# Kernel tuning notes

Measured on AMD Instinct MI355X. Metric: run time of the kernel, lower is better.

Reference implementation:

```python
import jax, jax.numpy as jnp
import numpy as np

EPS = 1e-5


def _extract3x3(x, stride=1):
    # channel-major patch extraction: output [B, C*9, Ho, Wo], each channel's 3x3 window contiguous
    B, C, H, W = x.shape
    xp = jnp.pad(x, ((0, 0), (0, 0), (1, 1), (1, 1)))
    Ho = (H + 2 - 3) // stride + 1
    Wo = (W + 2 - 3) // stride + 1
    pats = [xp[:, :, i:i + (Ho - 1) * stride + 1:stride, j:j + (Wo - 1) * stride + 1:stride]
            for i in range(3) for j in range(3)]
    return jnp.stack(pats, axis=2).reshape(B, C * 9, Ho, Wo)


def _amm(patches, centroids, lut, inv_temp):
    # patches: [B, D, H, W] channel-major, D = ncodebooks * subvec_len
    # centroids: [ncb, k, sub], lut: [ncb, k, out_channels]
    B, D, H, W = patches.shape
    ncb, k, sub = centroids.shape
    v = patches.reshape(B, ncb, sub, H * W).transpose(0, 3, 1, 2)  # [B, L, ncb, sub]
    # negative squared distance to each codeword (||v||^2 dropped: constant over k)
    scores = 2.0 * jnp.einsum('blcs,cks->blck', v, centroids) - jnp.sum(centroids * centroids, -1)[None, None]
    attn = jax.nn.softmax(scores * inv_temp, axis=-1)          # soft codeword assignment
    out = jnp.einsum('blck,cko->blo', attn, lut)                # LUT gather/sum over codebooks
    return out.transpose(0, 2, 1).reshape(B, -1, H, W)


def _bn(x, g, b):
    m = x.mean((0, 2, 3), keepdims=True)
    v = x.var((0, 2, 3), keepdims=True)
    return g[None, :, None, None] * (x - m) * jax.lax.rsqrt(v + EPS) + b[None, :, None, None]


def setup_inputs() -> dict:
    key = jax.random.key(0)
    ks = jax.random.split(key, 8)
    B, C, H, W = 32, 1024, 14, 14
    width, out_c, K = 256, 1024, 16
    return {
        'x': jax.random.normal(ks[0], (B, C, H, W), jnp.float32),
        'c1_centroids': jax.random.normal(ks[1], (C // 4, K, 4), jnp.float32),
        'c1_lut': jax.random.normal(ks[2], (C // 4, K, width), jnp.float32) * 0.05,
        'c1_invt': jnp.ones((), jnp.float32),
        'c2_centroids': jax.random.normal(ks[3], (width, K, 9), jnp.float32),
        'c2_lut': jax.random.normal(ks[4], (width, K, width), jnp.float32) * 0.05,
        'c2_invt': jnp.ones((), jnp.float32),
        'c3_centroids': jax.random.normal(ks[5], (width // 4, K, 4), jnp.float32),
        'c3_lut': jax.random.normal(ks[6], (width // 4, K, out_c), jnp.float32) * 0.05,
        'c3_invt': jnp.ones((), jnp.float32),
        'bn1_g': jnp.ones((width,), jnp.float32), 'bn1_b': jnp.zeros((width,), jnp.float32),
        'bn2_g': jnp.ones((width,), jnp.float32), 'bn2_b': jnp.zeros((width,), jnp.float32),
        'bn3_g': jnp.ones((out_c,), jnp.float32), 'bn3_b': jnp.zeros((out_c,), jnp.float32),
    }


def reference(x, c1_centroids, c1_lut, c1_invt, c2_centroids, c2_lut, c2_invt,
              c3_centroids, c3_lut, c3_invt, bn1_g, bn1_b, bn2_g, bn2_b, bn3_g, bn3_b):
    identity = x
    out = _amm(x, c1_centroids, c1_lut, c1_invt)                 # amm_conv1x1, stride 1
    out = jax.nn.relu(_bn(out, bn1_g, bn1_b))
    out = _amm(_extract3x3(out, 1), c2_centroids, c2_lut, c2_invt)  # amm_conv3x3, stride 1, pad 1
    out = jax.nn.relu(_bn(out, bn2_g, bn2_b))
    out = _amm(out, c3_centroids, c3_lut, c3_invt)               # amm_conv1x1
    out = _bn(out, bn3_g, bn3_b)
    return jax.nn.relu(out + identity)
```

## Files before the change

kernel.cpp:

```cpp
#include <hip/hip_runtime.h>
#include <hip/hip_bf16.h>

#define EPSV 1e-5f

typedef unsigned short u16;
typedef __attribute__((ext_vector_type(8))) short short8;
typedef __attribute__((ext_vector_type(4))) float f32x4;
typedef __hip_bfloat16 bf16;

__device__ __forceinline__ unsigned int pack2(float a, float b) {
  bf16 ha = __float2bfloat16(a), hb = __float2bfloat16(b);
  u16 ua, ub;
  __builtin_memcpy(&ua, &ha, 2);
  __builtin_memcpy(&ub, &hb, 2);
  return (unsigned int)ua | ((unsigned int)ub << 16);
}

typedef __attribute__((address_space(1))) const void gvoid_t;
typedef __attribute__((address_space(3))) void lvoid_t;
__device__ __forceinline__ void gload16(const void* g, void* l) {
  __builtin_amdgcn_global_load_lds((gvoid_t*)g, (lvoid_t*)l, 16, 0, 0);
}


__global__ __launch_bounds__(256) void prep_kernel(
    const float* __restrict__ x, const float* __restrict__ cent,
    const float* __restrict__ invt, u16* __restrict__ attn,
    const float* __restrict__ s1, bf16* __restrict__ d1,
    const float* __restrict__ s2, bf16* __restrict__ d2,
    const float* __restrict__ s3, bf16* __restrict__ d3)
{
  __shared__ __align__(16) float sh[7012];
  const int tid = threadIdx.x;
  if (blockIdx.x >= 1024) {
    const int bid = blockIdx.x - 1024;
    const int which = bid >> 8, sub = bid & 255;
    const float* in = (which == 0) ? s1 : (which == 1) ? s2 : s3;
    bf16* out = (which == 0) ? d1 : (which == 1) ? d2 : d3;
    const int K = (which == 2) ? 1024 : 4096;
    const int N = (which == 2) ? 1024 : 256;
    const int kt = K >> 6;
    const int bk = sub & (kt - 1), bn = sub / kt;
    const int k0 = bk * 64, n0 = bn * 64;
    float* t = sh;
    for (int idx = tid; idx < 4096; idx += 256) {
      int r = idx >> 6, c = idx & 63;
      t[r * 65 + c] = in[(size_t)(k0 + r) * N + n0 + c];
    }
    __syncthreads();
    for (int idx = tid; idx < 4096; idx += 256) {
      int r = idx >> 6, c = idx & 63;
      out[(size_t)(n0 + r) * K + k0 + c] = __float2bfloat16(t[c * 65 + r]);
    }
    return;
  }
  float* vs = sh;
  float* cs = sh + 6468;
  const int bi = blockIdx.x >> 5, cg = blockIdx.x & 31;
  const float* xb = x + ((size_t)bi * 1024 + cg * 32) * 196;
  for (int e = tid; e < 3136; e += 256) {
    int c = e / 98, p2 = e - c * 98;
    float2 w = *(const float2*)&xb[(size_t)c * 196 + p2 * 2];
    vs[(p2 * 2) * 33 + c] = w.x;
    vs[(p2 * 2 + 1) * 33 + c] = w.y;
  }
  if (tid < 128) {
    int cb = tid >> 4, kk = tid & 15;
    *(float4*)&cs[cb * 68 + kk * 4] =
        *(const float4*)&cent[(size_t)(cg * 8 + cb) * 64 + kk * 4];
  }
  __syncthreads();
  const float it = invt[0];
  const int cbL = tid & 7, pj = tid >> 3;
  float4 cv[16]; float cn[16];
  #pragma unroll
  for (int k = 0; k < 16; k++) {
    cv[k] = *(const float4*)&cs[cbL * 68 + k * 4];
    cn[k] = cv[k].x * cv[k].x + cv[k].y * cv[k].y + cv[k].z * cv[k].z + cv[k].w * cv[k].w;
  }
  for (int p = pj; p < 196; p += 32) {
    const float* vp = &vs[p * 33 + cbL * 4];
    const float v0 = vp[0], v1 = vp[1], v2 = vp[2], v3 = vp[3];
    float s[16], mx = -3e38f;
    #pragma unroll
    for (int k = 0; k < 16; k++) {
      float d = v0 * cv[k].x + v1 * cv[k].y + v2 * cv[k].z + v3 * cv[k].w;
      s[k] = it * (2.f * d - cn[k]);
      mx = fmaxf(mx, s[k]);
    }
    float sum = 0.f;
    #pragma unroll
    for (int k = 0; k < 16; k++) { float e = __expf(s[k] - mx); s[k] = e; sum += e; }
    const float r = 1.f / sum;
    uint4 w0, w1;
    w0.x = pack2(s[0] * r,  s[1] * r);  w0.y = pack2(s[2] * r,  s[3] * r);
    w0.z = pack2(s[4] * r,  s[5] * r);  w0.w = pack2(s[6] * r,  s[7] * r);
    w1.x = pack2(s[8] * r,  s[9] * r);  w1.y = pack2(s[10] * r, s[11] * r);
    w1.z = pack2(s[12] * r, s[13] * r); w1.w = pack2(s[14] * r, s[15] * r);
    uint4* dst = (uint4*)(attn + (size_t)(bi * 196 + p) * 4096 + (cg * 8 + cbL) * 16);
    dst[0] = w0; dst[1] = w1;
  }
}

__global__ __launch_bounds__(256) void attn2_kernel(const float* __restrict__ out1,
    const float* __restrict__ ss, const float* __restrict__ cent,
    const float* __restrict__ invt, u16* __restrict__ attn)
{
  __shared__ float vs[4 * 16 * 32];
  __shared__ __align__(16) float cs[32 * 196];
  const int tid = threadIdx.x;
  const int rp = blockIdx.x >> 3, cg = blockIdx.x & 7;
  const int b = rp / 7, y0 = (rp % 7) * 2, m0 = rp * 28;
  for (int e = tid; e < 2048; e += 256) {
    int c = e & 31, x1 = (e >> 5) & 15, dyy = e >> 9;
    int yy = y0 + dyy - 1, xx = x1 - 1;
    float v = 0.f;
    int ch = cg * 32 + c;
    if (yy >= 0 && yy < 14 && xx >= 0 && xx < 14) {
      float val = out1[(size_t)((b * 14 + yy) * 14 + xx) * 256 + ch];
      v = fmaxf(val * ss[ch] + ss[256 + ch], 0.f);
    }
    vs[e] = v;
  }
  for (int idx = tid; idx < 1152; idx += 256) {
    int cb = idx / 36, f4i = idx - cb * 36;
    float4 w = *(const float4*)&cent[(size_t)(cg * 32 + cb) * 144 + f4i * 4];
    int j0 = f4i * 4;
    #pragma unroll
    for (int t = 0; t < 4; t++) {
      int j = j0 + t, k = j / 9, jj = j - k * 9;
      cs[cb * 196 + k * 12 + jj] = ((const float*)&w)[t];
    }
  }
  __syncthreads();
  const float it = invt[0];
  const int cb = tid & 31, pq = tid >> 5;
  const int np = (pq < 4) ? 4 : 3;
  float v[4][9];
  #pragma unroll
  for (int i = 0; i < 4; i++) if (i < np) {
    const int p = i * 8 + pq;
    const int r = p / 14, xc = p - r * 14;
    #pragma unroll
    for (int dy = 0; dy < 3; dy++)
      #pragma unroll
      for (int dx = 0; dx < 3; dx++)
        v[i][dy * 3 + dx] = vs[((r + dy) * 16 + xc + dx) * 32 + cb];
  }
  float s[4][16];
  #pragma unroll
  for (int k = 0; k < 16; k++) {
    const float* ck = &cs[cb * 196 + k * 12];
    const float4 ca = *(const float4*)ck;
    const float4 cbv = *(const float4*)(ck + 4);
    const float c8 = ck[8];
    float c9[9] = {ca.x, ca.y, ca.z, ca.w, cbv.x, cbv.y, cbv.z, cbv.w, c8};
    float cn = 0.f;
    #pragma unroll
    for (int j = 0; j < 9; j++) cn = fmaf(c9[j], c9[j], cn);
    #pragma unroll
    for (int i = 0; i < 4; i++) if (i < np) {
      float d = 0.f;
      #pragma unroll
      for (int j = 0; j < 9; j++) d = fmaf(c9[j], v[i][j], d);
      s[i][k] = it * (2.f * d - cn);
    }
  }
  #pragma unroll
  for (int i = 0; i < 4; i++) if (i < np) {
    float mx = -3e38f;
    #pragma unroll
    for (int k = 0; k < 16; k++) mx = fmaxf(mx, s[i][k]);
    float sum = 0.f;
    #pragma unroll
    for (int k = 0; k < 16; k++) { float e = __expf(s[i][k] - mx); s[i][k] = e; sum += e; }
    const float r = 1.f / sum;
    uint4 w0, w1;
    w0.x = pack2(s[i][0] * r,  s[i][1] * r);  w0.y = pack2(s[i][2] * r,  s[i][3] * r);
    w0.z = pack2(s[i][4] * r,  s[i][5] * r);  w0.w = pack2(s[i][6] * r,  s[i][7] * r);
    w1.x = pack2(s[i][8] * r,  s[i][9] * r);  w1.y = pack2(s[i][10] * r, s[i][11] * r);
    w1.z = pack2(s[i][12] * r, s[i][13] * r); w1.w = pack2(s[i][14] * r, s[i][15] * r);
    uint4* dst = (uint4*)(attn + (size_t)(m0 + i * 8 + pq) * 4096 + (cg * 32 + cb) * 16);
    dst[0] = w0; dst[1] = w1;
  }
}

__global__ __launch_bounds__(256) void attn3_kernel(const float* __restrict__ out2,
    const float* __restrict__ ss, const float* __restrict__ cent,
    const float* __restrict__ invt, bf16* __restrict__ attn)
{
  const int t = threadIdx.x;
  const int cb = t & 63, ml = t >> 6;
  const int m0 = blockIdx.x * 16;
  const float it = invt[0];
  float4 cv[16]; float cn[16];
  const float4* cc = (const float4*)(cent + cb * 64);
  #pragma unroll
  for (int k = 0; k < 16; k++) {
    cv[k] = cc[k];
    cn[k] = cv[k].x * cv[k].x + cv[k].y * cv[k].y + cv[k].z * cv[k].z + cv[k].w * cv[k].w;
  }
  const float4 scv = *(const float4*)(ss + cb * 4);
  const float4 shv = *(const float4*)(ss + 256 + cb * 4);
  for (int g = 0; g < 4; g++) {
    const int m = m0 + g * 4 + ml;
    float4 xv = *(const float4*)(out2 + (size_t)m * 256 + cb * 4);
    float4 v;
    v.x = fmaxf(xv.x * scv.x + shv.x, 0.f);
    v.y = fmaxf(xv.y * scv.y + shv.y, 0.f);
    v.z = fmaxf(xv.z * scv.z + shv.z, 0.f);
    v.w = fmaxf(xv.w * scv.w + shv.w, 0.f);
    float s[16], mx = -3e38f;
    #pragma unroll
    for (int k = 0; k < 16; k++) {
      float d = v.x * cv[k].x + v.y * cv[k].y + v.z * cv[k].z + v.w * cv[k].w;
      s[k] = it * (2.f * d - cn[k]);
      mx = fmaxf(mx, s[k]);
    }
    float sum = 0.f;
    #pragma unroll
    for (int k = 0; k < 16; k++) { float e = __expf(s[k] - mx); s[k] = e; sum += e; }
    float r = 1.f / sum;
    #pragma unroll
    for (int k = 0; k < 16; k++)
      attn[(size_t)m * 1024 + cb * 16 + k] = __float2bfloat16(s[k] * r);
  }
}

template<int KDIM, int NT, int KSLICES, int BM, int BK>
__global__ __launch_bounds__(256) void gemm_kernel(const u16* __restrict__ A,
    const u16* __restrict__ Bt, float* __restrict__ C, size_t cstride)
{
  constexpr int NDIM = NT * 128;
  constexpr int KS = KDIM / KSLICES;
  constexpr int MT = 6272 / BM;
  constexpr int FM = BM / 32;
  constexpr int KU = BK / 32;
  constexpr int SLOTS = BK / 8;
  constexpr int RPC = 64 / SLOTS;
  constexpr int ACALLS = BM / (RPC * 4);
  constexpr int BCALLS = 128 / (RPC * 4);
  __shared__ __align__(16) u16 Asm[2][BM * BK];
  __shared__ __align__(16) u16 Bsm[2][128 * BK];
  const int tid = threadIdx.x;
  const int nt = blockIdx.x % NT;
  const int mt = (blockIdx.x / NT) % MT;
  const int sl = blockIdx.x / (NT * MT);
  const int kbeg = sl * KS, kend = kbeg + KS;
  const int m0 = mt * BM, n0 = nt * 128;
  const int lane = tid & 63, wid = tid >> 6;
  const int wm = wid >> 1, wn = wid & 1;
  const int lr = lane / SLOTS, sslot = lane % SLOTS;
  const int gs = sslot ^ (lr & 7);

  f32x4 acc[FM][4];
  #pragma unroll
  for (int i = 0; i < FM; i++)
    #pragma unroll
    for (int j = 0; j < 4; j++) acc[i][j] = (f32x4){0.f, 0.f, 0.f, 0.f};

  const u16* Abase = A + (size_t)m0 * KDIM;
  const u16* Bbase = Bt + (size_t)n0 * KDIM;

  auto stage = [&](int bf, int kb) {
    #pragma unroll
    for (int c = 0; c < ACALLS; c++) {
      const int r0 = (wid * ACALLS + c) * RPC;
      gload16(Abase + (size_t)(r0 + lr) * KDIM + kb + gs * 8, &Asm[bf][r0 * BK]);
    }
    #pragma unroll
    for (int c = 0; c < BCALLS; c++) {
      const int r0 = (wid * BCALLS + c) * RPC;
      gload16(Bbase + (size_t)(r0 + lr) * KDIM + kb + gs * 8, &Bsm[bf][r0 * BK]);
    }
  };

  auto compute = [&](int bf) {
    #pragma unroll
    for (int ks = 0; ks < KU; ks++) {
      short8 a[FM], b[4];
      #pragma unroll
      for (int f = 0; f < FM; f++) {
        const int ra = wm * (BM / 2) + f * 16 + (lane & 15);
        const int ja = (ks * 4 + (lane >> 4)) ^ (ra & 7);
        a[f] = *(const short8*)(&Asm[bf][ra * BK + ja * 8]);
      }
      #pragma unroll
      for (int f = 0; f < 4; f++) {
        const int rb = wn * 64 + f * 16 + (lane & 15);
        const int jb = (ks * 4 + (lane >> 4)) ^ (rb & 7);
        b[f] = *(const short8*)(&Bsm[bf][rb * BK + jb * 8]);
      }
      #pragma unroll
      for (int fm = 0; fm < FM; fm++)
        #pragma unroll
        for (int fn = 0; fn < 4; fn++)
          acc[fm][fn] = __builtin_amdgcn_mfma_f32_16x16x32_bf16(a[fm], b[fn], acc[fm][fn], 0, 0, 0);
    }
  };

  stage(0, kbeg);
  __syncthreads();
  int cur = 0;
  for (int kb = kbeg + BK; kb < kend; kb += BK) {
    stage(cur ^ 1, kb);
    compute(cur);
    __syncthreads();
    cur ^= 1;
  }
  compute(cur);

  float* __restrict__ Cs = C + (size_t)sl * cstride;
  #pragma unroll
  for (int fm = 0; fm < FM; fm++)
    #pragma unroll
    for (int fn = 0; fn < 4; fn++) {
      const int col = n0 + wn * 64 + fn * 16 + (lane & 15);
      const int rbase = m0 + wm * (BM / 2) + fm * 16 + (lane >> 4) * 4;
      #pragma unroll
      for (int r = 0; r < 4; r++)
        Cs[(size_t)(rbase + r) * NDIM + col] = acc[fm][fn][r];
    }
}

template<int CH, int NBLK, int NSUM>
__global__ __launch_bounds__(256) void bnpart_kernel(const float* __restrict__ buf,
    float* __restrict__ sum_out, float* __restrict__ part)
{
  constexpr int PC = CH / 256;
  constexpr int ROWS = 6272 / NBLK;
  constexpr size_t PSTR = 6272ull * CH;
  const int t = threadIdx.x, m0 = blockIdx.x * ROWS;
  float s[PC], s2[PC];
  #pragma unroll
  for (int j = 0; j < PC; j++) { s[j] = 0.f; s2[j] = 0.f; }
  for (int i = 0; i < ROWS; i++) {
    const size_t ro = (size_t)(m0 + i) * CH;
    #pragma unroll
    for (int j = 0; j < PC; j++) {
      float v = buf[ro + t + j * 256];
      #pragma unroll
      for (int n = 1; n < NSUM; n++) v += buf[(size_t)n * PSTR + ro + t + j * 256];
      if (NSUM > 1) sum_out[ro + t + j * 256] = v;
      s[j] += v; s2[j] = fmaf(v, v, s2[j]);
    }
  }
  #pragma unroll
  for (int j = 0; j < PC; j++) {
    part[(size_t)blockIdx.x * (2 * CH) + t + j * 256] = s[j];
    part[(size_t)blockIdx.x * (2 * CH) + CH + t + j * 256] = s2[j];
  }
}

template<int CH, int NBLK>
__global__ __launch_bounds__(256) void bnfin_kernel(const float* __restrict__ part,
    const float* __restrict__ g, const float* __restrict__ bb, float* __restrict__ ss)
{
  __shared__ float red[2][4][64];
  const int t = threadIdx.x;
  const int chl = t & 63, grp = t >> 6;
  const int c = blockIdx.x * 64 + chl;
  float S = 0.f, S2 = 0.f;
  for (int i = grp; i < NBLK; i += 4) {
    S += part[(size_t)i * (2 * CH) + c];
    S2 += part[(size_t)i * (2 * CH) + CH + c];
  }
  red[0][grp][chl] = S; red[1][grp][chl] = S2;
  __syncthreads();
  if (t < 64) {
    float Sf  = red[0][0][t] + red[0][1][t] + red[0][2][t] + red[0][3][t];
    float S2f = red[1][0][t] + red[1][1][t] + red[1][2][t] + red[1][3][t];
    const int ch = blockIdx.x * 64 + t;
    float mean = Sf * (1.f / 6272.f);
    float var = S2f * (1.f / 6272.f) - mean * mean;
    float sc = g[ch] * rsqrtf(var + EPSV);
    ss[ch] = sc;
    ss[CH + ch] = bb[ch] - mean * sc;
  }
}

__global__ __launch_bounds__(256) void tfinal_kernel(const float* __restrict__ out3,
    const float* __restrict__ ss, const float* __restrict__ x, float* __restrict__ out)
{
  __shared__ float t[64 * 199];
  const int b = blockIdx.x >> 4, n0 = (blockIdx.x & 15) * 64;
  for (int idx = threadIdx.x; idx < 196 * 64; idx += 256) {
    int p = idx >> 6, ni = idx & 63;
    float v = out3[(size_t)(b * 196 + p) * 1024 + n0 + ni] * ss[n0 + ni] + ss[1024 + n0 + ni];
    t[ni * 199 + p] = v;
  }
  __syncthreads();
  for (int idx = threadIdx.x; idx < 64 * 196; idx += 256) {
    int ni = idx / 196, p = idx - ni * 196;
    size_t o = (size_t)(b * 1024 + n0 + ni) * 196 + p;
    out[o] = fmaxf(t[ni * 199 + p] + x[o], 0.f);
  }
}


template<int CIN, int OUT, bool APPLY_BN>
__global__ __launch_bounds__(256) void amm1x1_kernel(
    const float* __restrict__ xin, const float* __restrict__ ss,
    const float* __restrict__ cent, const float* __restrict__ lut,
    const float* __restrict__ invt, float* __restrict__ outbuf)
{
  constexpr int NCB = CIN / 4;
  constexpr int NO = OUT / 256;
  __shared__ float vsm[CIN * 14];
  __shared__ __align__(16) float attn_sm[14 * 16];
  const int tid = threadIdx.x;
  const int b = blockIdx.x / 14, y = blockIdx.x % 14;
  const int rowbase = y * 14;
  for (int e = tid; e < CIN * 14; e += 256) {
    int c = e / 14, xc = e - c * 14;
    float v = xin[(b * CIN + c) * 196 + rowbase + xc];
    if (APPLY_BN) v = fmaxf(v * ss[c] + ss[CIN + c], 0.f);
    vsm[e] = v;
  }
  __syncthreads();
  float acc[14 * NO];
  #pragma unroll
  for (int i = 0; i < 14 * NO; i++) acc[i] = 0.f;
  const float it = invt[0];
  const int p_ = tid >> 4, k_ = tid & 15;
  for (int cb = 0; cb < NCB; ++cb) {
    if (tid < 224) {
      const float* cc = cent + (cb * 16 + k_) * 4;
      float s = 0.f;
      #pragma unroll
      for (int si = 0; si < 4; si++) {
        float cv = cc[si];
        float vv = vsm[(cb * 4 + si) * 14 + p_];
        s = fmaf(cv, 2.f * vv - cv, s);
      }
      s *= it;
      float m = s;
      #pragma unroll
      for (int off = 8; off; off >>= 1) m = fmaxf(m, __shfl_xor(m, off, 16));
      float e = __expf(s - m);
      float sum = e;
      #pragma unroll
      for (int off = 8; off; off >>= 1) sum += __shfl_xor(sum, off, 16);
      attn_sm[p_ * 16 + k_] = e / sum;
    }
    __syncthreads();
    float lv[NO][16];
    #pragma unroll
    for (int j = 0; j < NO; j++)
      #pragma unroll
      for (int k = 0; k < 16; k++)
        lv[j][k] = lut[(cb * 16 + k) * OUT + j * 256 + tid];
    const float4* a4 = (const float4*)attn_sm;
    #pragma unroll
    for (int p = 0; p < 14; p++) {
      float4 q0 = a4[p*4+0], q1 = a4[p*4+1], q2 = a4[p*4+2], q3 = a4[p*4+3];
      float av[16] = {q0.x,q0.y,q0.z,q0.w, q1.x,q1.y,q1.z,q1.w,
                      q2.x,q2.y,q2.z,q2.w, q3.x,q3.y,q3.z,q3.w};
      #pragma unroll
      for (int j = 0; j < NO; j++) {
        float s = acc[p * NO + j];
        #pragma unroll
        for (int k = 0; k < 16; k++) s = fmaf(av[k], lv[j][k], s);
        acc[p * NO + j] = s;
      }
    }
    __syncthreads();
  }
  #pragma unroll
  for (int j = 0; j < NO; j++) {
    int o = j * 256 + tid;
    #pragma unroll
    for (int p = 0; p < 14; p++)
      outbuf[(b * OUT + o) * 196 + rowbase + p] = acc[p * NO + j];
  }
}

__global__ __launch_bounds__(256) void amm3x3_kernel(
    const float* __restrict__ xin, const float* __restrict__ ss,
    const float* __restrict__ cent, const float* __restrict__ lut,
    const float* __restrict__ invt, float* __restrict__ outbuf)
{
  __shared__ float vsm[256 * 3 * 16];
  __shared__ __align__(16) float attn_sm[14 * 16];
  const int tid = threadIdx.x;
  const int b = blockIdx.x / 14, y = blockIdx.x % 14;
  for (int e = tid; e < 256 * 3 * 16; e += 256) {
    int c = e / 48, rem = e - c * 48, i = rem >> 4, col = rem & 15;
    int yy = y + i - 1, xx = col - 1;
    float v = 0.f;
    if (yy >= 0 && yy < 14 && xx >= 0 && xx < 14) {
      v = xin[(b * 256 + c) * 196 + yy * 14 + xx];
      v = fmaxf(v * ss[c] + ss[256 + c], 0.f);
    }
    vsm[e] = v;
  }
  __syncthreads();
  float acc[14];
  #pragma unroll
  for (int i = 0; i < 14; i++) acc[i] = 0.f;
  const float it = invt[0];
  const int p_ = tid >> 4, k_ = tid & 15;
  for (int cb = 0; cb < 256; ++cb) {
    if (tid < 224) {
      const float* cc = cent + (cb * 16 + k_) * 9;
      float s = 0.f;
      #pragma unroll
      for (int i = 0; i < 3; i++)
        #pragma unroll
        for (int j = 0; j < 3; j++) {
          float cv = cc[i * 3 + j];
          float vv = vsm[(cb * 3 + i) * 16 + p_ + j];
          s = fmaf(cv, 2.f * vv - cv, s);
        }
      s *= it;
      float m = s;
      #pragma unroll
      for (int off = 8; off; off >>= 1) m = fmaxf(m, __shfl_xor(m, off, 16));
      float e = __expf(s - m);
      float sum = e;
      #pragma unroll
      for (int off = 8; off; off >>= 1) sum += __shfl_xor(sum, off, 16);
      attn_sm[p_ * 16 + k_] = e / sum;
    }
    __syncthreads();
    float lv[16];
    #pragma unroll
    for (int k = 0; k < 16; k++) lv[k] = lut[(cb * 16 + k) * 256 + tid];
    const float4* a4 = (const float4*)attn_sm;
    #pragma unroll
    for (int p = 0; p < 14; p++) {
      float4 q0 = a4[p*4+0], q1 = a4[p*4+1], q2 = a4[p*4+2], q3 = a4[p*4+3];
      float av[16] = {q0.x,q0.y,q0.z,q0.w, q1.x,q1.y,q1.z,q1.w,
                      q2.x,q2.y,q2.z,q2.w, q3.x,q3.y,q3.z,q3.w};
      float s = acc[p];
      #pragma unroll
      for (int k = 0; k < 16; k++) s = fmaf(av[k], lv[k], s);
      acc[p] = s;
    }
    __syncthreads();
  }
  #pragma unroll
  for (int p = 0; p < 14; p++)
    outbuf[(b * 256 + tid) * 196 + y * 14 + p] = acc[p];
}

template<int CH>
__global__ __launch_bounds__(256) void bnstats_kernel(const float* __restrict__ buf,
    const float* __restrict__ g, const float* __restrict__ bb, float* __restrict__ ss)
{
  const int c = blockIdx.x, tid = threadIdx.x;
  float s = 0.f, s2 = 0.f;
  for (int e = tid; e < 32 * 196; e += 256) {
    int bi = e / 196, l = e - bi * 196;
    float v = buf[(bi * CH + c) * 196 + l];
    s += v; s2 = fmaf(v, v, s2);
  }
  #pragma unroll
  for (int off = 32; off; off >>= 1) { s += __shfl_down(s, off); s2 += __shfl_down(s2, off); }
  __shared__ float red[8];
  int w = tid >> 6;
  if ((tid & 63) == 0) { red[w] = s; red[4 + w] = s2; }
  __syncthreads();
  if (tid == 0) {
    float S  = red[0] + red[1] + red[2] + red[3];
    float S2 = red[4] + red[5] + red[6] + red[7];
    float mean = S * (1.f / 6272.f);
    float var  = S2 * (1.f / 6272.f) - mean * mean;
    float sc = g[c] * rsqrtf(var + EPSV);
    ss[c] = sc;
    ss[CH + c] = bb[c] - mean * sc;
  }
}

__global__ __launch_bounds__(256) void final_old_kernel(float* __restrict__ out3,
    const float* __restrict__ ss, const float* __restrict__ x)
{
  const int total = 32 * 1024 * 196;
  for (int idx = blockIdx.x * 256 + threadIdx.x; idx < total; idx += gridDim.x * 256) {
    int c = (idx / 196) & 1023;
    float v = out3[idx] * ss[c] + ss[1024 + c] + x[idx];
    out3[idx] = fmaxf(v, 0.f);
  }
}


extern "C" void kernel_launch(void* const* d_in, const int* in_sizes, int n_in,
                              void* d_out, int out_size, void* d_ws, size_t ws_size,
                              hipStream_t stream) {
  const float* x   = (const float*)d_in[0];
  const float* c1c = (const float*)d_in[1];
  const float* c1l = (const float*)d_in[2];
  const float* c1t = (const float*)d_in[3];
  const float* c2c = (const float*)d_in[4];
  const float* c2l = (const float*)d_in[5];
  const float* c2t = (const float*)d_in[6];
  const float* c3c = (const float*)d_in[7];
  const float* c3l = (const float*)d_in[8];
  const float* c3t = (const float*)d_in[9];
  const float* g1  = (const float*)d_in[10];
  const float* b1  = (const float*)d_in[11];
  const float* g2  = (const float*)d_in[12];
  const float* b2  = (const float*)d_in[13];
  const float* g3  = (const float*)d_in[14];
  const float* b3  = (const float*)d_in[15];

  float* ws = (float*)d_ws;
  const size_t FAST_NEED = 24255488ull * 4ull;

  if (ws_size >= FAST_NEED) {
    u16*   attnB = (u16*)ws;
    float* partC = ws + 12845056;
    float* out1  = partC + 6422528;
    float* out2  = out1 + 1605632;
    bf16*  lutT1 = (bf16*)(out2 + 1605632);
    bf16*  lutT2 = lutT1 + 1048576;
    bf16*  lutT3 = lutT2 + 1048576;
    float* part  = (float*)(lutT3 + 1048576);
    float* ss1   = part + 200704;
    float* ss2   = ss1 + 512;
    float* ss3   = ss2 + 512;
    float* out3  = partC;
    const size_t PART_STRIDE = 1605632;

    prep_kernel<<<1792, 256, 0, stream>>>(x, c1c, c1t, attnB,
                                          c1l, lutT1, c2l, lutT2, c3l, lutT3);

    gemm_kernel<4096, 2, 4, 128, 64><<<392, 256, 0, stream>>>(attnB, (const u16*)lutT1, partC, PART_STRIDE);
    bnpart_kernel<256, 196, 4><<<196, 256, 0, stream>>>(partC, out1, part);
    bnfin_kernel<256, 196><<<4, 256, 0, stream>>>(part, g1, b1, ss1);

    attn2_kernel<<<1792, 256, 0, stream>>>(out1, ss1, c2c, c2t, attnB);
    gemm_kernel<4096, 2, 4, 128, 64><<<392, 256, 0, stream>>>(attnB, (const u16*)lutT2, partC, PART_STRIDE);
    bnpart_kernel<256, 196, 4><<<196, 256, 0, stream>>>(partC, out2, part);
    bnfin_kernel<256, 196><<<4, 256, 0, stream>>>(part, g2, b2, ss2);

    attn3_kernel<<<392, 256, 0, stream>>>(out2, ss2, c3c, c3t, (bf16*)attnB);
    gemm_kernel<1024, 8, 1, 128, 64><<<392, 256, 0, stream>>>(attnB, (const u16*)lutT3, out3, 0);
    bnpart_kernel<1024, 98, 1><<<98, 256, 0, stream>>>(out3, nullptr, part);
    bnfin_kernel<1024, 98><<<16, 256, 0, stream>>>(part, g3, b3, ss3);

    tfinal_kernel<<<512, 256, 0, stream>>>(out3, ss3, x, (float*)d_out);
  } else {
    float* out3 = (float*)d_out;
    float* out1 = ws;
    float* out2 = out1 + 32 * 256 * 196;
    float* ss1  = out2 + 32 * 256 * 196;
    float* ss2  = ss1 + 512;
    float* ss3  = ss2 + 512;

    amm1x1_kernel<1024, 256, false><<<448, 256, 0, stream>>>(x, nullptr, c1c, c1l, c1t, out1);
    bnstats_kernel<256><<<256, 256, 0, stream>>>(out1, g1, b1, ss1);
    amm3x3_kernel<<<448, 256, 0, stream>>>(out1, ss1, c2c, c2l, c2t, out2);
    bnstats_kernel<256><<<256, 256, 0, stream>>>(out2, g2, b2, ss2);
    amm1x1_kernel<256, 1024, true><<<448, 256, 0, stream>>>(out2, ss2, c3c, c3l, c3t, out3);
    bnstats_kernel<1024><<<1024, 256, 0, stream>>>(out3, g3, b3, ss3);
    final_old_kernel<<<2048, 256, 0, stream>>>(out3, ss3, x);
  }
}
```

Baseline: 318.1 us.

## Fold BN finalize into consumer kernels via atomic stats and remap GEMM blocks

Drops the three separate bnfin launches. bnpart now atomically adds per-channel sums and sums of squares into small accumulators, which block 0 of the preceding GEMM zeroes. Each consumer kernel (attn2, attn3, tfinal) recomputes its channels' scale and shift from those sums into shared memory. Separately, the GEMM remaps block indices in an XCD-interleaved order when the grid size is a multiple of 8, to improve cache locality across dies. The trade-offs are float atomic contention, a non-deterministic summation order, and redundant small per-block stat computations.

```diff
diff --git a/kernel.cpp b/kernel.cpp
--- a/kernel.cpp
+++ b/kernel.cpp
@@ -103,14 +103,25 @@
 }
 
 __global__ __launch_bounds__(256) void attn2_kernel(const float* __restrict__ out1,
-    const float* __restrict__ ss, const float* __restrict__ cent,
+    const float* __restrict__ g, const float* __restrict__ bb,
+    const float* __restrict__ Sacc, const float* __restrict__ cent,
     const float* __restrict__ invt, u16* __restrict__ attn)
 {
   __shared__ float vs[4 * 16 * 32];
   __shared__ __align__(16) float cs[32 * 196];
+  __shared__ float ssl[64];
   const int tid = threadIdx.x;
   const int rp = blockIdx.x >> 3, cg = blockIdx.x & 7;
   const int b = rp / 7, y0 = (rp % 7) * 2, m0 = rp * 28;
+  if (tid < 32) {
+    const int ch = cg * 32 + tid;
+    float S = Sacc[ch], S2 = Sacc[256 + ch];
+    float mean = S * (1.f / 6272.f);
+    float var = S2 * (1.f / 6272.f) - mean * mean;
+    float sc = g[ch] * rsqrtf(var + EPSV);
+    ssl[tid] = sc; ssl[32 + tid] = bb[ch] - mean * sc;
+  }
+  __syncthreads();
   for (int e = tid; e < 2048; e += 256) {
     int c = e & 31, x1 = (e >> 5) & 15, dyy = e >> 9;
     int yy = y0 + dyy - 1, xx = x1 - 1;
@@ -118,7 +129,7 @@
     int ch = cg * 32 + c;
     if (yy >= 0 && yy < 14 && xx >= 0 && xx < 14) {
       float val = out1[(size_t)((b * 14 + yy) * 14 + xx) * 256 + ch];
-      v = fmaxf(val * ss[ch] + ss[256 + ch], 0.f);
+      v = fmaxf(val * ssl[c] + ssl[32 + c], 0.f);
     }
     vs[e] = v;
   }
@@ -186,10 +197,20 @@
 }
 
 __global__ __launch_bounds__(256) void attn3_kernel(const float* __restrict__ out2,
-    const float* __restrict__ ss, const float* __restrict__ cent,
+    const float* __restrict__ g, const float* __restrict__ bb,
+    const float* __restrict__ Sacc, const float* __restrict__ cent,
     const float* __restrict__ invt, bf16* __restrict__ attn)
 {
+  __shared__ float ssl[512];
   const int t = threadIdx.x;
+  {
+    float S = Sacc[t], S2 = Sacc[256 + t];
+    float mean = S * (1.f / 6272.f);
+    float var = S2 * (1.f / 6272.f) - mean * mean;
+    float sc = g[t] * rsqrtf(var + EPSV);
+    ssl[t] = sc; ssl[256 + t] = bb[t] - mean * sc;
+  }
+  __syncthreads();
   const int cb = t & 63, ml = t >> 6;
   const int m0 = blockIdx.x * 16;
   const float it = invt[0];
@@ -200,10 +221,10 @@
     cv[k] = cc[k];
     cn[k] = cv[k].x * cv[k].x + cv[k].y * cv[k].y + cv[k].z * cv[k].z + cv[k].w * cv[k].w;
   }
-  const float4 scv = *(const float4*)(ss + cb * 4);
-  const float4 shv = *(const float4*)(ss + 256 + cb * 4);
-  for (int g = 0; g < 4; g++) {
-    const int m = m0 + g * 4 + ml;
+  const float4 scv = *(const float4*)(ssl + cb * 4);
+  const float4 shv = *(const float4*)(ssl + 256 + cb * 4);
+  for (int gi = 0; gi < 4; gi++) {
+    const int m = m0 + gi * 4 + ml;
     float4 xv = *(const float4*)(out2 + (size_t)m * 256 + cb * 4);
     float4 v;
     v.x = fmaxf(xv.x * scv.x + shv.x, 0.f);
@@ -229,7 +250,8 @@
 
 template<int KDIM, int NT, int KSLICES, int BM, int BK>
 __global__ __launch_bounds__(256) void gemm_kernel(const u16* __restrict__ A,
-    const u16* __restrict__ Bt, float* __restrict__ C, size_t cstride)
+    const u16* __restrict__ Bt, float* __restrict__ C, size_t cstride,
+    float* __restrict__ zacc, int zn)
 {
   constexpr int NDIM = NT * 128;
   constexpr int KS = KDIM / KSLICES;
@@ -243,9 +265,15 @@
   __shared__ __align__(16) u16 Asm[2][BM * BK];
   __shared__ __align__(16) u16 Bsm[2][128 * BK];
   const int tid = threadIdx.x;
-  const int nt = blockIdx.x % NT;
-  const int mt = (blockIdx.x / NT) % MT;
-  const int sl = blockIdx.x / (NT * MT);
+  if (blockIdx.x == 0 && zacc) {
+    for (int i = tid; i < zn; i += 256) zacc[i] = 0.f;
+  }
+  const int nwg = gridDim.x;
+  int wg = blockIdx.x;
+  if ((nwg & 7) == 0) wg = (blockIdx.x & 7) * (nwg >> 3) + (blockIdx.x >> 3);
+  const int nt = wg % NT;
+  const int mt = (wg / NT) % MT;
+  const int sl = wg / (NT * MT);
   const int kbeg = sl * KS, kend = kbeg + KS;
   const int m0 = mt * BM, n0 = nt * 128;
   const int lane = tid & 63, wid = tid >> 6;
@@ -325,7 +353,7 @@
 
 template<int CH, int NBLK, int NSUM>
 __global__ __launch_bounds__(256) void bnpart_kernel(const float* __restrict__ buf,
-    float* __restrict__ sum_out, float* __restrict__ part)
+    float* __restrict__ sum_out, float* __restrict__ acc)
 {
   constexpr int PC = CH / 256;
   constexpr int ROWS = 6272 / NBLK;
@@ -347,46 +375,31 @@
   }
   #pragma unroll
   for (int j = 0; j < PC; j++) {
-    part[(size_t)blockIdx.x * (2 * CH) + t + j * 256] = s[j];
-    part[(size_t)blockIdx.x * (2 * CH) + CH + t + j * 256] = s2[j];
-  }
-}
-
-template<int CH, int NBLK>
-__global__ __launch_bounds__(256) void bnfin_kernel(const float* __restrict__ part,
-    const float* __restrict__ g, const float* __restrict__ bb, float* __restrict__ ss)
-{
-  __shared__ float red[2][4][64];
-  const int t = threadIdx.x;
-  const int chl = t & 63, grp = t >> 6;
-  const int c = blockIdx.x * 64 + chl;
-  float S = 0.f, S2 = 0.f;
-  for (int i = grp; i < NBLK; i += 4) {
-    S += part[(size_t)i * (2 * CH) + c];
-    S2 += part[(size_t)i * (2 * CH) + CH + c];
-  }
-  red[0][grp][chl] = S; red[1][grp][chl] = S2;
-  __syncthreads();
-  if (t < 64) {
-    float Sf  = red[0][0][t] + red[0][1][t] + red[0][2][t] + red[0][3][t];
-    float S2f = red[1][0][t] + red[1][1][t] + red[1][2][t] + red[1][3][t];
-    const int ch = blockIdx.x * 64 + t;
-    float mean = Sf * (1.f / 6272.f);
-    float var = S2f * (1.f / 6272.f) - mean * mean;
+    atomicAdd(&acc[t + j * 256], s[j]);
+    atomicAdd(&acc[CH + t + j * 256], s2[j]);
+  }
+}
+
+__global__ __launch_bounds__(256) void tfinal_kernel(const float* __restrict__ out3,
+    const float* __restrict__ g, const float* __restrict__ bb,
+    const float* __restrict__ Sacc, const float* __restrict__ x,
+    float* __restrict__ out)
+{
+  __shared__ float t[64 * 199];
+  __shared__ float ssl[128];
+  const int b = blockIdx.x >> 4, n0 = (blockIdx.x & 15) * 64;
+  if (threadIdx.x < 64) {
+    const int ch = n0 + threadIdx.x;
+    float S = Sacc[ch], S2 = Sacc[1024 + ch];
+    float mean = S * (1.f / 6272.f);
+    float var = S2 * (1.f / 6272.f) - mean * mean;
     float sc = g[ch] * rsqrtf(var + EPSV);
-    ss[ch] = sc;
-    ss[CH + ch] = bb[ch] - mean * sc;
-  }
-}
-
-__global__ __launch_bounds__(256) void tfinal_kernel(const float* __restrict__ out3,
-    const float* __restrict__ ss, const float* __restrict__ x, float* __restrict__ out)
-{
-  __shared__ float t[64 * 199];
-  const int b = blockIdx.x >> 4, n0 = (blockIdx.x & 15) * 64;
+    ssl[threadIdx.x] = sc; ssl[64 + threadIdx.x] = bb[ch] - mean * sc;
+  }
+  __syncthreads();
   for (int idx = threadIdx.x; idx < 196 * 64; idx += 256) {
     int p = idx >> 6, ni = idx & 63;
-    float v = out3[(size_t)(b * 196 + p) * 1024 + n0 + ni] * ss[n0 + ni] + ss[1024 + n0 + ni];
+    float v = out3[(size_t)(b * 196 + p) * 1024 + n0 + ni] * ssl[ni] + ssl[64 + ni];
     t[ni * 199 + p] = v;
   }
   __syncthreads();
@@ -615,31 +628,30 @@
     bf16*  lutT1 = (bf16*)(out2 + 1605632);
     bf16*  lutT2 = lutT1 + 1048576;
     bf16*  lutT3 = lutT2 + 1048576;
-    float* part  = (float*)(lutT3 + 1048576);
-    float* ss1   = part + 200704;
-    float* ss2   = ss1 + 512;
-    float* ss3   = ss2 + 512;
+    float* acc1  = (float*)(lutT3 + 1048576);
+    float* acc2  = acc1 + 512;
+    float* acc3  = acc2 + 512;
     float* out3  = partC;
     const size_t PART_STRIDE = 1605632;
 
     prep_kernel<<<1792, 256, 0, stream>>>(x, c1c, c1t, attnB,
                                           c1l, lutT1, c2l, lutT2, c3l, lutT3);
 
-    gemm_kernel<4096, 2, 4, 128, 64><<<392, 256, 0, stream>>>(attnB, (const u16*)lutT1, partC, PART_STRIDE);
-    bnpart_kernel<256, 196, 4><<<196, 256, 0, stream>>>(partC, out1, part);
-    bnfin_kernel<256, 196><<<4, 256, 0, stream>>>(part, g1, b1, ss1);
-
-    attn2_kernel<<<1792, 256, 0, stream>>>(out1, ss1, c2c, c2t, attnB);
-    gemm_kernel<4096, 2, 4, 128, 64><<<392, 256, 0, stream>>>(attnB, (const u16*)lutT2, partC, PART_STRIDE);
-    bnpart_kernel<256, 196, 4><<<196, 256, 0, stream>>>(partC, out2, part);
-    bnfin_kernel<256, 196><<<4, 256, 0, stream>>>(part, g2, b2, ss2);
-
-    attn3_kernel<<<392, 256, 0, stream>>>(out2, ss2, c3c, c3t, (bf16*)attnB);
-    gemm_kernel<1024, 8, 1, 128, 64><<<392, 256, 0, stream>>>(attnB, (const u16*)lutT3, out3, 0);
-    bnpart_kernel<1024, 98, 1><<<98, 256, 0, stream>>>(out3, nullptr, part);
-    bnfin_kernel<1024, 98><<<16, 256, 0, stream>>>(part, g3, b3, ss3);
-
-    tfinal_kernel<<<512, 256, 0, stream>>>(out3, ss3, x, (float*)d_out);
+    gemm_kernel<4096, 2, 4, 128, 64><<<392, 256, 0, stream>>>(
+        attnB, (const u16*)lutT1, partC, PART_STRIDE, acc1, 512);
+    bnpart_kernel<256, 196, 4><<<196, 256, 0, stream>>>(partC, out1, acc1);
+
+    attn2_kernel<<<1792, 256, 0, stream>>>(out1, g1, b1, acc1, c2c, c2t, attnB);
+    gemm_kernel<4096, 2, 4, 128, 64><<<392, 256, 0, stream>>>(
+        attnB, (const u16*)lutT2, partC, PART_STRIDE, acc2, 512);
+    bnpart_kernel<256, 196, 4><<<196, 256, 0, stream>>>(partC, out2, acc2);
+
+    attn3_kernel<<<392, 256, 0, stream>>>(out2, g2, b2, acc2, c3c, c3t, (bf16*)attnB);
+    gemm_kernel<1024, 8, 1, 128, 64><<<392, 256, 0, stream>>>(
+        attnB, (const u16*)lutT3, out3, 0, acc3, 2048);
+    bnpart_kernel<1024, 98, 1><<<98, 256, 0, stream>>>(out3, nullptr, acc3);
+
+    tfinal_kernel<<<512, 256, 0, stream>>>(out3, g3, b3, acc3, x, (float*)d_out);
   } else {
     float* out3 = (float*)d_out;
     float* out1 = ws;
```

Measured after the change: 292.2 us. 8.2% less time.
